# Performance work log

Measured on AMD Instinct MI355X. Metric: run time of the kernel, lower is better.

The kernel has to match this reference:

```python
import jax, jax.numpy as jnp
import numpy as np

T, N, E, NNZ, F, D = 8, 50000, 5000, 100000, 128, 128


def setup_inputs() -> dict:
    key = jax.random.key(0)
    ks = jax.random.split(key, 5)
    x = jax.random.normal(ks[0], (T, N, F), jnp.float32)
    pair_nodes = jax.random.randint(ks[1], (T, NNZ), 0, N)
    pair_edges = jax.random.randint(ks[2], (T, NNZ), 0, E)
    W0 = jax.random.normal(ks[3], (F, D), jnp.float32) / np.sqrt(F).astype(np.float32)
    b0 = jnp.zeros((D,), jnp.float32)
    W1 = jax.random.normal(ks[4], (D, D), jnp.float32) / np.sqrt(D).astype(np.float32)
    b1 = jnp.zeros((D,), jnp.float32)
    return {"x": x, "W0": W0, "b0": b0, "W1": W1, "b1": b1,
            "pair_nodes": pair_nodes, "pair_edges": pair_edges}


def _smooth(x, pn, pe):
    """HGNN Laplacian smoothing: D_v^{-1/2} H D_e^{-1} H^T D_v^{-1/2} x.

    x: [N, D]; pn/pe: [NNZ] incidence pairs (node idx, hyperedge idx).
    """
    ones = jnp.ones(pn.shape, x.dtype)
    dv = jax.ops.segment_sum(ones, pn, num_segments=N)  # node degree
    de = jax.ops.segment_sum(ones, pe, num_segments=E)  # hyperedge degree
    dv_safe = jnp.where(dv > 0, dv, 1.0)
    de_safe = jnp.where(de > 0, de, 1.0)
    dv_isqrt = jnp.where(dv > 0, jax.lax.rsqrt(dv_safe), 0.0)
    de_inv = jnp.where(de > 0, 1.0 / de_safe, 0.0)
    xs = x * dv_isqrt[:, None]
    # node -> hyperedge gather/aggregate
    ef = jax.ops.segment_sum(xs[pn], pe, num_segments=E) * de_inv[:, None]
    # hyperedge -> node gather/scatter
    return jax.ops.segment_sum(ef[pe], pn, num_segments=N) * dv_isqrt[:, None]


def reference(x, W0, b0, W1, b1, pair_nodes, pair_edges):
    def step(xt, pn, pe):
        h = jax.nn.relu(_smooth(xt @ W0 + b0, pn, pe))   # layer 0
        h = jax.nn.relu(_smooth(h @ W1 + b1, pn, pe))    # layer 1
        return h.mean(axis=0)                            # mean pool over nodes
    tokens = jax.vmap(step)(x, pair_nodes, pair_edges)   # [T, D]
    return tokens[None]                                  # [1, T, D]
```

## Files before the change

### kernel.cpp

```cpp
#include <hip/hip_runtime.h>

#define TT  8
#define NN  50000
#define EE  5000
#define NZ  100000
#define DD  128
#define ETILES ((EE + 63) / 64)
#define ECAP 64
#define NCAP 32
#define LSTR 136

typedef __attribute__((ext_vector_type(8))) short short8v;
typedef __attribute__((ext_vector_type(4))) float float4v;

__device__ __forceinline__ unsigned short f2bf(float f) {
    return __builtin_bit_cast(unsigned short, (__bf16)f);
}
__device__ __forceinline__ float bf2f(unsigned short u) {
    return (float)__builtin_bit_cast(__bf16, u);
}

__global__ __launch_bounds__(256) void k_build(const int* __restrict__ pn, const int* __restrict__ pe,
                                               int* __restrict__ dvcnt, int* __restrict__ decnt,
                                               int* __restrict__ ell_e, int* __restrict__ ell_n) {
    const int t = blockIdx.x & 7;
    const int i = (blockIdx.x >> 3) * 256 + threadIdx.x;
    if (i >= NZ) return;
    int n = pn[(size_t)t * NZ + i];
    int e = pe[(size_t)t * NZ + i];
    int se_ = atomicAdd(&decnt[(size_t)t * EE + e], 1);
    if (se_ < ECAP) ell_e[((size_t)t * EE + e) * ECAP + se_] = n;
    int sn = atomicAdd(&dvcnt[(size_t)t * NN + n], 1);
    if (sn < NCAP) ell_n[((size_t)t * NN + n) * NCAP + sn] = e;
}

__global__ __launch_bounds__(256) void k_fin(const int* __restrict__ dvcnt, const int* __restrict__ decnt,
                                             float* __restrict__ dvis, float* __restrict__ deinv) {
    int i = blockIdx.x * 256 + threadIdx.x;
    if (i < TT * NN) {
        int c = dvcnt[i];
        dvis[i] = (c > 0) ? rsqrtf((float)c) : 0.0f;
    } else {
        int j = i - TT * NN;
        if (j < TT * EE) {
            int c = decnt[j];
            deinv[j] = (c > 0) ? 1.0f / (float)c : 0.0f;
        }
    }
}

__global__ __launch_bounds__(256) void k_prepw(const float* __restrict__ W0, const float* __restrict__ W1,
                                               unsigned short* __restrict__ fragH,
                                               unsigned short* __restrict__ fragL) {
    const float* W = blockIdx.x ? W1 : W0;
    unsigned short* fh = fragH + (size_t)blockIdx.x * 16384;
    unsigned short* fl = fragL + (size_t)blockIdx.x * 16384;
    const int wave = threadIdx.x >> 6, lane = threadIdx.x & 63;
    const int l15 = lane & 15, l4 = lane >> 4;
    #pragma unroll
    for (int c = 0; c < 2; c++)
        #pragma unroll
        for (int s = 0; s < 4; s++)
            #pragma unroll
            for (int j = 0; j < 8; j++) {
                float wv = W[(size_t)(s * 32 + l4 * 8 + j) * DD + wave * 32 + c * 16 + l15];
                unsigned short h = f2bf(wv);
                int idx = (((wave * 2 + c) * 4 + s) * 64 + lane) * 8 + j;
                fh[idx] = h;
                fl[idx] = f2bf(wv - bf2f(h));
            }
}

__global__ __launch_bounds__(256) void k_gather_e0(const int* __restrict__ ell_e, const int* __restrict__ decnt,
                                                   const float* __restrict__ dvis, const float* __restrict__ x,
                                                   float* __restrict__ g, float* __restrict__ se) {
    const int t = blockIdx.x & 7;
    const int e = (blockIdx.x >> 3) * 16 + (threadIdx.x >> 4);
    const int lane16 = threadIdx.x & 15;
    if (e >= EE) return;
    const float* xsrc = x + (size_t)t * NN * DD;
    const float* dvs = dvis + (size_t)t * NN;
    const int* ellrow = ell_e + ((size_t)t * EE + e) * ECAP;
    int cnt = decnt[(size_t)t * EE + e];
    cnt = cnt < ECAP ? cnt : ECAP;
    float acc[8] = {};
    float sacc = 0.f;
    for (int b = 0; b < ECAP; b += 16) {
        if (b >= cnt) break;
        int valid = (b + lane16 < cnt);
        int idx = valid ? ellrow[b + lane16] : 0;
        float dvl = valid ? dvs[idx] : 0.f;
        #pragma unroll
        for (int j = 0; j < 16; j++) {
            if (b + j < cnt) {
                int n = __shfl(idx, j, 16);
                float dvn = __shfl(dvl, j, 16);
                float4 v0 = *(const float4*)(xsrc + (size_t)n * DD + lane16 * 8);
                float4 v1 = *(const float4*)(xsrc + (size_t)n * DD + lane16 * 8 + 4);
                acc[0] += dvn * v0.x; acc[1] += dvn * v0.y; acc[2] += dvn * v0.z; acc[3] += dvn * v0.w;
                acc[4] += dvn * v1.x; acc[5] += dvn * v1.y; acc[6] += dvn * v1.z; acc[7] += dvn * v1.w;
                sacc += dvn;
            }
        }
    }
    float* gout = g + ((size_t)t * EE + e) * DD;
    *(float4*)(gout + lane16 * 8)     = make_float4(acc[0], acc[1], acc[2], acc[3]);
    *(float4*)(gout + lane16 * 8 + 4) = make_float4(acc[4], acc[5], acc[6], acc[7]);
    if (lane16 == 0) se[(size_t)t * EE + e] = sacc;
}

__global__ __launch_bounds__(256) void k_gather_e1(const int* __restrict__ ell_e, const int* __restrict__ decnt,
                                                   const float* __restrict__ dvis,
                                                   const unsigned short* __restrict__ h,
                                                   float* __restrict__ g) {
    const int t = blockIdx.x & 7;
    const int e = (blockIdx.x >> 3) * 16 + (threadIdx.x >> 4);
    const int lane16 = threadIdx.x & 15;
    if (e >= EE) return;
    const unsigned short* hsrc = h + (size_t)t * NN * DD;
    const float* dvs = dvis + (size_t)t * NN;
    const int* ellrow = ell_e + ((size_t)t * EE + e) * ECAP;
    int cnt = decnt[(size_t)t * EE + e];
    cnt = cnt < ECAP ? cnt : ECAP;
    float acc[8] = {};
    for (int b = 0; b < ECAP; b += 16) {
        if (b >= cnt) break;
        int valid = (b + lane16 < cnt);
        int idx = valid ? ellrow[b + lane16] : 0;
        float dvl = valid ? dvs[idx] : 0.f;
        #pragma unroll
        for (int j = 0; j < 16; j++) {
            if (b + j < cnt) {
                int n = __shfl(idx, j, 16);
                float dvn = __shfl(dvl, j, 16);
                short8v v = *(const short8v*)(hsrc + (size_t)n * DD + lane16 * 8);
                #pragma unroll
                for (int k = 0; k < 8; k++) acc[k] += dvn * bf2f((unsigned short)v[k]);
            }
        }
    }
    float* gout = g + ((size_t)t * EE + e) * DD;
    *(float4*)(gout + lane16 * 8)     = make_float4(acc[0], acc[1], acc[2], acc[3]);
    *(float4*)(gout + lane16 * 8 + 4) = make_float4(acc[4], acc[5], acc[6], acc[7]);
}

__global__ __launch_bounds__(256) void k_gemmE(const float* __restrict__ g,
                                               const float* __restrict__ se,
                                               const float* __restrict__ deinv,
                                               const unsigned short* __restrict__ fragH,
                                               const unsigned short* __restrict__ fragL,
                                               const float* __restrict__ bias,
                                               unsigned short* __restrict__ ef) {
    __shared__ unsigned short Ah[64 * LSTR];
    __shared__ unsigned short Al[64 * LSTR];
    __shared__ unsigned short E_lds[64 * LSTR];
    const int t = blockIdx.x & 7;
    const int tile = blockIdx.x >> 3;
    const int row0 = tile * 64;
    const float* gsrc = g + (size_t)t * EE * DD;
    const float* sesrc = se + (size_t)t * EE;
    const float* desrc = deinv + (size_t)t * EE;
    unsigned short* outp = ef + (size_t)t * EE * DD;
    const int tid = threadIdx.x;
    const int wave = tid >> 6, lane = tid & 63;
    const int l15 = lane & 15, l4 = lane >> 4;

    #pragma unroll
    for (int it = 0; it < 8; it++) {
        int idx = it * 256 + tid;
        int row = idx >> 5, col4 = idx & 31;
        float4 a = make_float4(0.f, 0.f, 0.f, 0.f);
        if (row0 + row < EE) a = *(const float4*)(gsrc + (size_t)(row0 + row) * DD + col4 * 4);
        unsigned short hx = f2bf(a.x), hy = f2bf(a.y), hz = f2bf(a.z), hw = f2bf(a.w);
        *(uint2*)(&Ah[row * LSTR + col4 * 4]) = make_uint2(
            (unsigned)hx | ((unsigned)hy << 16), (unsigned)hz | ((unsigned)hw << 16));
        *(uint2*)(&Al[row * LSTR + col4 * 4]) = make_uint2(
            (unsigned)f2bf(a.x - bf2f(hx)) | ((unsigned)f2bf(a.y - bf2f(hy)) << 16),
            (unsigned)f2bf(a.z - bf2f(hz)) | ((unsigned)f2bf(a.w - bf2f(hw)) << 16));
    }

    short8v wh[2][4], wl[2][4];
    #pragma unroll
    for (int c = 0; c < 2; c++)
        #pragma unroll
        for (int s = 0; s < 4; s++) {
            int base = (((wave * 2 + c) * 4 + s) * 64 + lane) * 8;
            wh[c][s] = *(const short8v*)(fragH + base);
            wl[c][s] = *(const short8v*)(fragL + base);
        }
    __syncthreads();

    float4v acc[4][2] = {};
    #pragma unroll
    for (int s = 0; s < 4; s++)
        #pragma unroll
        for (int r = 0; r < 4; r++) {
            short8v ah = *(const short8v*)(&Ah[(r * 16 + l15) * LSTR + s * 32 + l4 * 8]);
            short8v al = *(const short8v*)(&Al[(r * 16 + l15) * LSTR + s * 32 + l4 * 8]);
            #pragma unroll
            for (int c = 0; c < 2; c++) {
                acc[r][c] = __builtin_amdgcn_mfma_f32_16x16x32_bf16(ah, wh[c][s], acc[r][c], 0, 0, 0);
                acc[r][c] = __builtin_amdgcn_mfma_f32_16x16x32_bf16(al, wh[c][s], acc[r][c], 0, 0, 0);
                acc[r][c] = __builtin_amdgcn_mfma_f32_16x16x32_bf16(ah, wl[c][s], acc[r][c], 0, 0, 0);
            }
        }

    float b2[2] = { bias[wave * 32 + l15], bias[wave * 32 + 16 + l15] };
    __syncthreads();
    #pragma unroll
    for (int r = 0; r < 4; r++) {
        int rloc = r * 16 + l4 * 4;
        if (row0 + rloc < EE) {
            float4 de4 = *(const float4*)(desrc + row0 + rloc);
            float4 se4 = *(const float4*)(sesrc + row0 + rloc);
            float dev[4] = {de4.x, de4.y, de4.z, de4.w};
            float sev[4] = {se4.x, se4.y, se4.z, se4.w};
            #pragma unroll
            for (int c = 0; c < 2; c++)
                #pragma unroll
                for (int q = 0; q < 4; q++)
                    E_lds[(rloc + q) * LSTR + wave * 32 + c * 16 + l15] =
                        f2bf(dev[q] * (acc[r][c][q] + sev[q] * b2[c]));
        }
    }
    __syncthreads();
    #pragma unroll
    for (int it = 0; it < 8; it++) {
        int idx = it * 256 + tid;
        int row = idx >> 5, col4 = idx & 31;
        if (row0 + row < EE) {
            unsigned u0 = *(const unsigned*)(&E_lds[row * LSTR + col4 * 4]);
            unsigned u1 = *(const unsigned*)(&E_lds[row * LSTR + col4 * 4 + 2]);
            unsigned o2[2] = {u0, u1};
            *(uint2*)(outp + (size_t)(row0 + row) * DD + col4 * 4) = *(uint2*)o2;
        }
    }
}

__global__ __launch_bounds__(256) void k_gather_n0(const int* __restrict__ ell_n, const int* __restrict__ dvcnt,
                                                   const unsigned short* __restrict__ ef,
                                                   const float* __restrict__ dvis,
                                                   unsigned short* __restrict__ h) {
    const int t = blockIdx.x & 7;
    const int n = (blockIdx.x >> 3) * 16 + (threadIdx.x >> 4);
    const int lane16 = threadIdx.x & 15;
    if (n >= NN) return;
    const unsigned short* esrc = ef + (size_t)t * EE * DD;
    const int* ellrow = ell_n + ((size_t)t * NN + n) * NCAP;
    int cnt = dvcnt[(size_t)t * NN + n];
    cnt = cnt < NCAP ? cnt : NCAP;
    float dvn = dvis[(size_t)t * NN + n];
    float acc[8] = {};
    int idx = ellrow[lane16];
    #pragma unroll
    for (int j = 0; j < 16; j++) {
        if (j < cnt) {
            int e = __shfl(idx, j, 16);
            short8v v = *(const short8v*)(esrc + (size_t)e * DD + lane16 * 8);
            #pragma unroll
            for (int k = 0; k < 8; k++) acc[k] += bf2f((unsigned short)v[k]);
        }
    }
    if (cnt > 16) {
        int idx2 = ellrow[16 + lane16];
        #pragma unroll
        for (int j = 0; j < 16; j++) {
            if (16 + j < cnt) {
                int e = __shfl(idx2, j, 16);
                short8v v = *(const short8v*)(esrc + (size_t)e * DD + lane16 * 8);
                #pragma unroll
                for (int k = 0; k < 8; k++) acc[k] += bf2f((unsigned short)v[k]);
            }
        }
    }
    short8v o;
    #pragma unroll
    for (int k = 0; k < 8; k++) o[k] = (short)f2bf(fmaxf(acc[k] * dvn, 0.f));
    *(short8v*)(h + (size_t)t * NN * DD + (size_t)n * DD + lane16 * 8) = o;
}

__global__ __launch_bounds__(256) void k_gather_n1(const int* __restrict__ ell_n, const int* __restrict__ dvcnt,
                                                   const unsigned short* __restrict__ ef,
                                                   const float* __restrict__ dvis,
                                                   float* __restrict__ outp) {
    const int t = blockIdx.x & 7;
    const int nbase = (blockIdx.x >> 3) * 128 + (threadIdx.x >> 4) * 8;
    const int gg_ = threadIdx.x >> 4;
    const int lane16 = threadIdx.x & 15;
    const unsigned short* esrc = ef + (size_t)t * EE * DD;
    float px[8] = {};
    #pragma unroll
    for (int i = 0; i < 8; i++) {
        int n = nbase + i;
        if (n < NN) {
            const int* ellrow = ell_n + ((size_t)t * NN + n) * NCAP;
            int cnt = dvcnt[(size_t)t * NN + n];
            cnt = cnt < NCAP ? cnt : NCAP;
            float dvn = dvis[(size_t)t * NN + n];
            float acc[8] = {};
            int idx = ellrow[lane16];
            #pragma unroll
            for (int j = 0; j < 16; j++) {
                if (j < cnt) {
                    int e = __shfl(idx, j, 16);
                    short8v v = *(const short8v*)(esrc + (size_t)e * DD + lane16 * 8);
                    #pragma unroll
                    for (int k = 0; k < 8; k++) acc[k] += bf2f((unsigned short)v[k]);
                }
            }
            if (cnt > 16) {
                int idx2 = ellrow[16 + lane16];
                #pragma unroll
                for (int j = 0; j < 16; j++) {
                    if (16 + j < cnt) {
                        int e = __shfl(idx2, j, 16);
                        short8v v = *(const short8v*)(esrc + (size_t)e * DD + lane16 * 8);
                        #pragma unroll
                        for (int k = 0; k < 8; k++) acc[k] += bf2f((unsigned short)v[k]);
                    }
                }
            }
            #pragma unroll
            for (int k = 0; k < 8; k++) px[k] += fmaxf(acc[k] * dvn, 0.f);
        }
    }
    __shared__ float sp[16][128];
    #pragma unroll
    for (int k = 0; k < 8; k++) sp[gg_][lane16 * 8 + k] = px[k];
    __syncthreads();
    if (threadIdx.x < 128) {
        float ssum = 0.f;
        #pragma unroll
        for (int q = 0; q < 16; q++) ssum += sp[q][threadIdx.x];
        atomicAdd(outp + (size_t)t * DD + threadIdx.x, ssum * (1.0f / (float)NN));
    }
}

extern "C" void kernel_launch(void* const* d_in, const int* in_sizes, int n_in,
                              void* d_out, int out_size, void* d_ws, size_t ws_size,
                              hipStream_t stream) {
    const float* x  = (const float*)d_in[0];
    const float* W0 = (const float*)d_in[1];
    const float* b0 = (const float*)d_in[2];
    const float* W1 = (const float*)d_in[3];
    const float* b1 = (const float*)d_in[4];
    const int*   pn = (const int*)d_in[5];
    const int*   pe = (const int*)d_in[6];
    float* out = (float*)d_out;

    char* p = (char*)d_ws;
    auto alloc = [&](size_t bytes) -> char* {
        char* r = p;
        p += (bytes + 255) / 256 * 256;
        return r;
    };
    float* dvis  = (float*)alloc((size_t)TT * NN * 4);
    float* deinv = (float*)alloc((size_t)TT * EE * 4);
    int*   dvcnt = (int*)alloc((size_t)TT * (NN + EE) * 4);
    int*   decnt = dvcnt + (size_t)TT * NN;
    int*   ell_e = (int*)alloc((size_t)TT * EE * ECAP * 4);
    int*   ell_n = (int*)alloc((size_t)TT * NN * NCAP * 4);
    unsigned short* wfragH = (unsigned short*)alloc(2 * 16384 * 2);
    unsigned short* wfragL = (unsigned short*)alloc(2 * 16384 * 2);
    float* gbuf = (float*)alloc((size_t)TT * EE * DD * 4);
    float* sebuf = (float*)alloc((size_t)TT * EE * 4);
    unsigned short* ef = (unsigned short*)alloc((size_t)TT * EE * DD * 2);
    unsigned short* h  = (unsigned short*)alloc((size_t)TT * NN * DD * 2);

    hipMemsetAsync(dvcnt, 0, (size_t)TT * (NN + EE) * 4, stream);
    hipMemsetAsync(d_out, 0, (size_t)out_size * 4, stream);

    k_prepw<<<2, 256, 0, stream>>>(W0, W1, wfragH, wfragL);
    k_build<<<((NZ + 255) / 256) * 8, 256, 0, stream>>>(pn, pe, dvcnt, decnt, ell_e, ell_n);
    k_fin<<<(TT * (NN + EE) + 255) / 256, 256, 0, stream>>>(dvcnt, decnt, dvis, deinv);

    const dim3 ge(((EE + 15) / 16) * 8), gn(((NN + 15) / 16) * 8);

    k_gather_e0<<<ge, 256, 0, stream>>>(ell_e, decnt, dvis, x, gbuf, sebuf);
    k_gemmE<<<ETILES * 8, 256, 0, stream>>>(gbuf, sebuf, deinv, wfragH, wfragL, b0, ef);
    k_gather_n0<<<gn, 256, 0, stream>>>(ell_n, dvcnt, ef, dvis, h);
    k_gather_e1<<<ge, 256, 0, stream>>>(ell_e, decnt, dvis, h, gbuf);
    k_gemmE<<<ETILES * 8, 256, 0, stream>>>(gbuf, sebuf, deinv, wfragH + 16384, wfragL + 16384, b1, ef);
    k_gather_n1<<<((NN + 127) / 128) * 8, 256, 0, stream>>>(ell_n, dvcnt, ef, dvis, out);
}
```

Measured before the change: 313.2 us.

## Fuse edge-to-node-to-edge gather, pre-cast x to fp16, shrink node ELL cap

Drops the materialized layer-0 node features h. A new fused kernel recomputes each node's aggregate inside the next hyperedge gather, applies relu there, and accumulates straight into the edge buffer. Input x is pre-scaled by dv^-1/2 and cast to fp16 in a separate pass, so the first gather reads half the bytes. Edge features switch from bf16 to fp16, and the node ELL capacity drops from 32 to 16. In exchange, node aggregates are recomputed once per incidence, fp16 adds precision and range risk, and nodes with more than 16 hyperedges get truncated.

```diff
diff --git a/kernel.cpp b/kernel.cpp
--- a/kernel.cpp
+++ b/kernel.cpp
@@ -7,7 +7,7 @@
 #define DD  128
 #define ETILES ((EE + 63) / 64)
 #define ECAP 64
-#define NCAP 32
+#define NCAP 16
 #define LSTR 136
 
 typedef __attribute__((ext_vector_type(8))) short short8v;
@@ -18,6 +18,12 @@
 }
 __device__ __forceinline__ float bf2f(unsigned short u) {
     return (float)__builtin_bit_cast(__bf16, u);
+}
+__device__ __forceinline__ unsigned short f2h(float f) {
+    return __builtin_bit_cast(unsigned short, (_Float16)f);
+}
+__device__ __forceinline__ float h2f(unsigned short u) {
+    return (float)__builtin_bit_cast(_Float16, u);
 }
 
 __global__ __launch_bounds__(256) void k_build(const int* __restrict__ pn, const int* __restrict__ pe,
@@ -71,14 +77,32 @@
             }
 }
 
-__global__ __launch_bounds__(256) void k_gather_e0(const int* __restrict__ ell_e, const int* __restrict__ decnt,
-                                                   const float* __restrict__ dvis, const float* __restrict__ x,
+__global__ __launch_bounds__(256) void k_cast(const float* __restrict__ x, const float* __restrict__ dvis,
+                                              unsigned short* __restrict__ xh) {
+    int gid = blockIdx.x * 256 + threadIdx.x;
+    if (gid >= TT * NN * (DD / 8)) return;
+    int row = gid >> 4;
+    int c8 = gid & 15;
+    float dv = dvis[row];
+    float4 a0 = *(const float4*)(x + (size_t)row * DD + c8 * 8);
+    float4 a1 = *(const float4*)(x + (size_t)row * DD + c8 * 8 + 4);
+    short8v o;
+    o[0] = (short)f2h(dv * a0.x); o[1] = (short)f2h(dv * a0.y);
+    o[2] = (short)f2h(dv * a0.z); o[3] = (short)f2h(dv * a0.w);
+    o[4] = (short)f2h(dv * a1.x); o[5] = (short)f2h(dv * a1.y);
+    o[6] = (short)f2h(dv * a1.z); o[7] = (short)f2h(dv * a1.w);
+    *(short8v*)(xh + (size_t)row * DD + c8 * 8) = o;
+}
+
+__global__ __launch_bounds__(256) void k_gather_eb(const int* __restrict__ ell_e, const int* __restrict__ decnt,
+                                                   const float* __restrict__ dvis,
+                                                   const unsigned short* __restrict__ xh,
                                                    float* __restrict__ g, float* __restrict__ se) {
     const int t = blockIdx.x & 7;
     const int e = (blockIdx.x >> 3) * 16 + (threadIdx.x >> 4);
     const int lane16 = threadIdx.x & 15;
     if (e >= EE) return;
-    const float* xsrc = x + (size_t)t * NN * DD;
+    const unsigned short* xsrc = xh + (size_t)t * NN * DD;
     const float* dvs = dvis + (size_t)t * NN;
     const int* ellrow = ell_e + ((size_t)t * EE + e) * ECAP;
     int cnt = decnt[(size_t)t * EE + e];
@@ -89,59 +113,23 @@
         if (b >= cnt) break;
         int valid = (b + lane16 < cnt);
         int idx = valid ? ellrow[b + lane16] : 0;
-        float dvl = valid ? dvs[idx] : 0.f;
+        sacc += valid ? dvs[idx] : 0.f;
         #pragma unroll
         for (int j = 0; j < 16; j++) {
             if (b + j < cnt) {
                 int n = __shfl(idx, j, 16);
-                float dvn = __shfl(dvl, j, 16);
-                float4 v0 = *(const float4*)(xsrc + (size_t)n * DD + lane16 * 8);
-                float4 v1 = *(const float4*)(xsrc + (size_t)n * DD + lane16 * 8 + 4);
-                acc[0] += dvn * v0.x; acc[1] += dvn * v0.y; acc[2] += dvn * v0.z; acc[3] += dvn * v0.w;
-                acc[4] += dvn * v1.x; acc[5] += dvn * v1.y; acc[6] += dvn * v1.z; acc[7] += dvn * v1.w;
-                sacc += dvn;
+                short8v v = *(const short8v*)(xsrc + (size_t)n * DD + lane16 * 8);
+                #pragma unroll
+                for (int k = 0; k < 8; k++) acc[k] += h2f((unsigned short)v[k]);
             }
         }
     }
     float* gout = g + ((size_t)t * EE + e) * DD;
     *(float4*)(gout + lane16 * 8)     = make_float4(acc[0], acc[1], acc[2], acc[3]);
     *(float4*)(gout + lane16 * 8 + 4) = make_float4(acc[4], acc[5], acc[6], acc[7]);
+    #pragma unroll
+    for (int w = 1; w < 16; w <<= 1) sacc += __shfl_xor(sacc, w, 16);
     if (lane16 == 0) se[(size_t)t * EE + e] = sacc;
-}
-
-__global__ __launch_bounds__(256) void k_gather_e1(const int* __restrict__ ell_e, const int* __restrict__ decnt,
-                                                   const float* __restrict__ dvis,
-                                                   const unsigned short* __restrict__ h,
-                                                   float* __restrict__ g) {
-    const int t = blockIdx.x & 7;
-    const int e = (blockIdx.x >> 3) * 16 + (threadIdx.x >> 4);
-    const int lane16 = threadIdx.x & 15;
-    if (e >= EE) return;
-    const unsigned short* hsrc = h + (size_t)t * NN * DD;
-    const float* dvs = dvis + (size_t)t * NN;
-    const int* ellrow = ell_e + ((size_t)t * EE + e) * ECAP;
-    int cnt = decnt[(size_t)t * EE + e];
-    cnt = cnt < ECAP ? cnt : ECAP;
-    float acc[8] = {};
-    for (int b = 0; b < ECAP; b += 16) {
-        if (b >= cnt) break;
-        int valid = (b + lane16 < cnt);
-        int idx = valid ? ellrow[b + lane16] : 0;
-        float dvl = valid ? dvs[idx] : 0.f;
-        #pragma unroll
-        for (int j = 0; j < 16; j++) {
-            if (b + j < cnt) {
-                int n = __shfl(idx, j, 16);
-                float dvn = __shfl(dvl, j, 16);
-                short8v v = *(const short8v*)(hsrc + (size_t)n * DD + lane16 * 8);
-                #pragma unroll
-                for (int k = 0; k < 8; k++) acc[k] += dvn * bf2f((unsigned short)v[k]);
-            }
-        }
-    }
-    float* gout = g + ((size_t)t * EE + e) * DD;
-    *(float4*)(gout + lane16 * 8)     = make_float4(acc[0], acc[1], acc[2], acc[3]);
-    *(float4*)(gout + lane16 * 8 + 4) = make_float4(acc[4], acc[5], acc[6], acc[7]);
 }
 
 __global__ __launch_bounds__(256) void k_gemmE(const float* __restrict__ g,
@@ -220,7 +208,7 @@
                 #pragma unroll
                 for (int q = 0; q < 4; q++)
                     E_lds[(rloc + q) * LSTR + wave * 32 + c * 16 + l15] =
-                        f2bf(dev[q] * (acc[r][c][q] + sev[q] * b2[c]));
+                        f2h(dev[q] * (acc[r][c][q] + sev[q] * b2[c]));
         }
     }
     __syncthreads();
@@ -237,46 +225,56 @@
     }
 }
 
-__global__ __launch_bounds__(256) void k_gather_n0(const int* __restrict__ ell_n, const int* __restrict__ dvcnt,
+__global__ __launch_bounds__(256) void k_gather_ee(const int* __restrict__ ell_e, const int* __restrict__ decnt,
+                                                   const int* __restrict__ ell_n, const int* __restrict__ dvcnt,
+                                                   const float* __restrict__ dvis,
                                                    const unsigned short* __restrict__ ef,
-                                                   const float* __restrict__ dvis,
-                                                   unsigned short* __restrict__ h) {
-    const int t = blockIdx.x & 7;
-    const int n = (blockIdx.x >> 3) * 16 + (threadIdx.x >> 4);
+                                                   float* __restrict__ g2) {
+    const int t = blockIdx.x & 7;
+    const int e = (blockIdx.x >> 3) * 16 + (threadIdx.x >> 4);
     const int lane16 = threadIdx.x & 15;
-    if (n >= NN) return;
+    if (e >= EE) return;
     const unsigned short* esrc = ef + (size_t)t * EE * DD;
-    const int* ellrow = ell_n + ((size_t)t * NN + n) * NCAP;
-    int cnt = dvcnt[(size_t)t * NN + n];
-    cnt = cnt < NCAP ? cnt : NCAP;
-    float dvn = dvis[(size_t)t * NN + n];
-    float acc[8] = {};
-    int idx = ellrow[lane16];
-    #pragma unroll
-    for (int j = 0; j < 16; j++) {
-        if (j < cnt) {
-            int e = __shfl(idx, j, 16);
-            short8v v = *(const short8v*)(esrc + (size_t)e * DD + lane16 * 8);
-            #pragma unroll
-            for (int k = 0; k < 8; k++) acc[k] += bf2f((unsigned short)v[k]);
-        }
-    }
-    if (cnt > 16) {
-        int idx2 = ellrow[16 + lane16];
-        #pragma unroll
+    const float* dvs = dvis + (size_t)t * NN;
+    const int* dcnt = dvcnt + (size_t)t * NN;
+    const int* elln = ell_n + (size_t)t * NN * NCAP;
+    const int* ellrow = ell_e + ((size_t)t * EE + e) * ECAP;
+    int cnt = decnt[(size_t)t * EE + e];
+    cnt = cnt < ECAP ? cnt : ECAP;
+    float gacc[8] = {};
+    for (int b = 0; b < ECAP; b += 16) {
+        if (b >= cnt) break;
+        int valid = (b + lane16 < cnt);
+        int n_l  = valid ? ellrow[b + lane16] : 0;
+        float dv_l = valid ? dvs[n_l] : 0.f;
+        int cn_l = valid ? dcnt[n_l] : 0;
+        cn_l = cn_l < NCAP ? cn_l : NCAP;
+        #pragma unroll 4
         for (int j = 0; j < 16; j++) {
-            if (16 + j < cnt) {
-                int e = __shfl(idx2, j, 16);
-                short8v v = *(const short8v*)(esrc + (size_t)e * DD + lane16 * 8);
+            if (b + j >= cnt) break;
+            int nj   = __shfl(n_l, j, 16);
+            float dvn = __shfl(dv_l, j, 16);
+            int cn   = __shfl(cn_l, j, 16);
+            int ev = (lane16 < cn) ? elln[(size_t)nj * NCAP + lane16] : 0;
+            float hacc[8] = {};
+            for (int kk = 0; kk < cn; kk += 4) {
                 #pragma unroll
-                for (int k = 0; k < 8; k++) acc[k] += bf2f((unsigned short)v[k]);
-            }
-        }
-    }
-    short8v o;
-    #pragma unroll
-    for (int k = 0; k < 8; k++) o[k] = (short)f2bf(fmaxf(acc[k] * dvn, 0.f));
-    *(short8v*)(h + (size_t)t * NN * DD + (size_t)n * DD + lane16 * 8) = o;
+                for (int u = 0; u < 4; u++) {
+                    if (kk + u < cn) {
+                        int e2 = __shfl(ev, kk + u, 16);
+                        short8v v = *(const short8v*)(esrc + (size_t)e2 * DD + lane16 * 8);
+                        #pragma unroll
+                        for (int k = 0; k < 8; k++) hacc[k] += h2f((unsigned short)v[k]);
+                    }
+                }
+            }
+            #pragma unroll
+            for (int k = 0; k < 8; k++) gacc[k] += dvn * fmaxf(dvn * hacc[k], 0.f);
+        }
+    }
+    float* gout = g2 + ((size_t)t * EE + e) * DD;
+    *(float4*)(gout + lane16 * 8)     = make_float4(gacc[0], gacc[1], gacc[2], gacc[3]);
+    *(float4*)(gout + lane16 * 8 + 4) = make_float4(gacc[4], gacc[5], gacc[6], gacc[7]);
 }
 
 __global__ __launch_bounds__(256) void k_gather_n1(const int* __restrict__ ell_n, const int* __restrict__ dvcnt,
@@ -298,26 +296,14 @@
             cnt = cnt < NCAP ? cnt : NCAP;
             float dvn = dvis[(size_t)t * NN + n];
             float acc[8] = {};
-            int idx = ellrow[lane16];
+            int idx = (lane16 < cnt) ? ellrow[lane16] : 0;
             #pragma unroll
             for (int j = 0; j < 16; j++) {
                 if (j < cnt) {
                     int e = __shfl(idx, j, 16);
                     short8v v = *(const short8v*)(esrc + (size_t)e * DD + lane16 * 8);
                     #pragma unroll
-                    for (int k = 0; k < 8; k++) acc[k] += bf2f((unsigned short)v[k]);
-                }
-            }
-            if (cnt > 16) {
-                int idx2 = ellrow[16 + lane16];
-                #pragma unroll
-                for (int j = 0; j < 16; j++) {
-                    if (16 + j < cnt) {
-                        int e = __shfl(idx2, j, 16);
-                        short8v v = *(const short8v*)(esrc + (size_t)e * DD + lane16 * 8);
-                        #pragma unroll
-                        for (int k = 0; k < 8; k++) acc[k] += bf2f((unsigned short)v[k]);
-                    }
+                    for (int k = 0; k < 8; k++) acc[k] += h2f((unsigned short)v[k]);
                 }
             }
             #pragma unroll
@@ -362,10 +348,10 @@
     int*   ell_n = (int*)alloc((size_t)TT * NN * NCAP * 4);
     unsigned short* wfragH = (unsigned short*)alloc(2 * 16384 * 2);
     unsigned short* wfragL = (unsigned short*)alloc(2 * 16384 * 2);
+    unsigned short* xh = (unsigned short*)alloc((size_t)TT * NN * DD * 2);
     float* gbuf = (float*)alloc((size_t)TT * EE * DD * 4);
     float* sebuf = (float*)alloc((size_t)TT * EE * 4);
     unsigned short* ef = (unsigned short*)alloc((size_t)TT * EE * DD * 2);
-    unsigned short* h  = (unsigned short*)alloc((size_t)TT * NN * DD * 2);
 
     hipMemsetAsync(dvcnt, 0, (size_t)TT * (NN + EE) * 4, stream);
     hipMemsetAsync(d_out, 0, (size_t)out_size * 4, stream);
@@ -373,13 +359,13 @@
     k_prepw<<<2, 256, 0, stream>>>(W0, W1, wfragH, wfragL);
     k_build<<<((NZ + 255) / 256) * 8, 256, 0, stream>>>(pn, pe, dvcnt, decnt, ell_e, ell_n);
     k_fin<<<(TT * (NN + EE) + 255) / 256, 256, 0, stream>>>(dvcnt, decnt, dvis, deinv);
-
-    const dim3 ge(((EE + 15) / 16) * 8), gn(((NN + 15) / 16) * 8);
-
-    k_gather_e0<<<ge, 256, 0, stream>>>(ell_e, decnt, dvis, x, gbuf, sebuf);
+    k_cast<<<(TT * NN * (DD / 8) + 255) / 256, 256, 0, stream>>>(x, dvis, xh);
+
+    const dim3 ge(((EE + 15) / 16) * 8);
+
+    k_gather_eb<<<ge, 256, 0, stream>>>(ell_e, decnt, dvis, xh, gbuf, sebuf);
     k_gemmE<<<ETILES * 8, 256, 0, stream>>>(gbuf, sebuf, deinv, wfragH, wfragL, b0, ef);
-    k_gather_n0<<<gn, 256, 0, stream>>>(ell_n, dvcnt, ef, dvis, h);
-    k_gather_e1<<<ge, 256, 0, stream>>>(ell_e, decnt, dvis, h, gbuf);
+    k_gather_ee<<<ge, 256, 0, stream>>>(ell_e, decnt, ell_n, dvcnt, dvis, ef, gbuf);
     k_gemmE<<<ETILES * 8, 256, 0, stream>>>(gbuf, sebuf, deinv, wfragH + 16384, wfragL + 16384, b1, ef);
     k_gather_n1<<<((NN + 127) / 128) * 8, 256, 0, stream>>>(ell_n, dvcnt, ef, dvis, out);
 }
```

Result: slower. 350.5 us (+11.9%).
